# Kernel optimization log

Hardware: AMD Instinct MI355X
Metric: run time of the kernel (lower is better)

The kernel has to match this reference:

```python
import jax, jax.numpy as jnp
import numpy as np

M = 8192          # flattened tokens (batch*seq)
IN_FEATURES = 4096
OUT_FEATURES = 4096


def setup_inputs() -> dict:
    key = jax.random.key(0)
    k1, k2, k3 = jax.random.split(key, 3)
    # int8-valued activations and weights, stored as int32 (values in [-128, 127])
    x = jax.random.randint(k1, (M, IN_FEATURES), -128, 128, dtype=jnp.int32)
    int_weight = jax.random.randint(k2, (OUT_FEATURES, IN_FEATURES), -128, 127, dtype=jnp.int32)
    bias = (jax.random.normal(k3, (OUT_FEATURES,), dtype=jnp.float32) * 0.02).astype(jnp.float16)
    return {"x": x, "int_weight": int_weight, "bias": bias}


def reference(x, int_weight, bias):
    # x.to(torch.int8); quik int8Matmul: int8 GEMM with int32 accumulation, out = x @ W^T
    x_i8 = x.astype(jnp.int8)
    w_i8 = int_weight.astype(jnp.int8)
    acc = jax.lax.dot_general(
        x_i8, w_i8,
        dimension_numbers=(((1,), (1,)), ((), ())),  # [M, K] x [N, K] -> [M, N]
        preferred_element_type=jnp.int32,
    )
    # .to(torch.float16) then bias add (fused epilogue target)
    return acc.astype(jnp.float16) + bias
```

## Files before the change

kernel.cpp:

```cpp
#include <hip/hip_runtime.h>

#define MDIM 8192
#define NDIM 4096
#define KDIM 4096
#define BM 256
#define BN 128
#define BK 64

typedef int v4i __attribute__((ext_vector_type(4)));
typedef int v16i __attribute__((ext_vector_type(16)));

__device__ __forceinline__ unsigned pack4(int x, int y, int z, int w) {
    return (unsigned)(x & 0xff) | ((unsigned)(y & 0xff) << 8) |
           ((unsigned)(z & 0xff) << 16) | ((unsigned)w << 24);
}

__global__ __launch_bounds__(256) void pack_i32_to_i8(const int* __restrict__ in,
                                                      unsigned* __restrict__ out) {
    const int i = blockIdx.x * 256 + threadIdx.x;
    const int4* p = (const int4*)in + (size_t)i * 4;
    int4 a = p[0], b = p[1], c = p[2], d = p[3];
    uint4 r;
    r.x = pack4(a.x, a.y, a.z, a.w);
    r.y = pack4(b.x, b.y, b.z, b.w);
    r.z = pack4(c.x, c.y, c.z, c.w);
    r.w = pack4(d.x, d.y, d.z, d.w);
    ((uint4*)out)[i] = r;
}

template <bool PACKED>
__global__ __launch_bounds__(256, 2) void gemm_i8(const char* __restrict__ Ap,
                                                  const char* __restrict__ Bp,
                                                  const int* __restrict__ A32,
                                                  const int* __restrict__ B32,
                                                  const _Float16* __restrict__ bias,
                                                  _Float16* __restrict__ out) {
    __shared__ char lds[24576];
    char* ldsA = lds;
    char* ldsB = lds + 16384;

    const int tid  = threadIdx.x;
    const int lane = tid & 63;
    const int wave = tid >> 6;
    const int bm0 = blockIdx.y * BM;
    const int bn0 = blockIdx.x * BN;

    int aoffs[4], boffs[2];
    char* adst[4];
    char* bdst[2];
#pragma unroll
    for (int r = 0; r < 4; ++r) {
        const int flat = (r * 4 + wave) * 1024 + lane * 16;
        const int row  = flat >> 6;
        const int fblk = ((flat >> 4) & 3) ^ ((row >> 1) & 3);
        aoffs[r] = (bm0 + row) * KDIM + fblk * 16;
        adst[r]  = ldsA + (r * 4 + wave) * 1024;
    }
#pragma unroll
    for (int r = 0; r < 2; ++r) {
        const int flat = (r * 4 + wave) * 1024 + lane * 16;
        const int row  = flat >> 6;
        const int fblk = ((flat >> 4) & 3) ^ ((row >> 1) & 3);
        boffs[r] = (bn0 + row) * KDIM + fblk * 16;
        bdst[r]  = ldsB + (r * 4 + wave) * 1024;
    }

    const int wr  = wave >> 1;
    const int wc  = wave & 1;
    const int l31 = lane & 31;
    const int kg  = lane >> 5;
    int aaddr[4][2], baddr[2][2];
#pragma unroll
    for (int mt = 0; mt < 4; ++mt) {
        const int row = wr * 128 + mt * 32 + l31;
        const int swz = (row >> 1) & 3;
#pragma unroll
        for (int ks = 0; ks < 2; ++ks) {
            const int kb = ks * 2 + kg;
            aaddr[mt][ks] = row * 64 + ((kb ^ swz) << 4);
        }
    }
#pragma unroll
    for (int nt = 0; nt < 2; ++nt) {
        const int row = wc * 64 + nt * 32 + l31;
        const int swz = (row >> 1) & 3;
#pragma unroll
        for (int ks = 0; ks < 2; ++ks) {
            const int kb = ks * 2 + kg;
            baddr[nt][ks] = 16384 + row * 64 + ((kb ^ swz) << 4);
        }
    }

    v16i acc[4][2];
#pragma unroll
    for (int mt = 0; mt < 4; ++mt)
#pragma unroll
        for (int nt = 0; nt < 2; ++nt)
#pragma unroll
            for (int i = 0; i < 16; ++i) acc[mt][nt][i] = 0;

    for (int k0 = 0; k0 < KDIM; k0 += BK) {
        if constexpr (PACKED) {
#pragma unroll
            for (int r = 0; r < 4; ++r) {
                __builtin_amdgcn_global_load_lds(
                    (__attribute__((address_space(1))) void*)(Ap + aoffs[r]),
                    (__attribute__((address_space(3))) void*)(adst[r]), 16, 0, 0);
                aoffs[r] += BK;
            }
#pragma unroll
            for (int r = 0; r < 2; ++r) {
                __builtin_amdgcn_global_load_lds(
                    (__attribute__((address_space(1))) void*)(Bp + boffs[r]),
                    (__attribute__((address_space(3))) void*)(bdst[r]), 16, 0, 0);
                boffs[r] += BK;
            }
        } else {
#pragma unroll
            for (int r = 0; r < 4; ++r) {
                const int flat = (r * 4 + wave) * 1024 + lane * 16;
                const int row  = flat >> 6;
                const int fblk = ((flat >> 4) & 3) ^ ((row >> 1) & 3);
                const int* src = A32 + (size_t)(bm0 + row) * KDIM + k0 + fblk * 16;
                int4 v0 = ((const int4*)src)[0], v1 = ((const int4*)src)[1];
                int4 v2 = ((const int4*)src)[2], v3 = ((const int4*)src)[3];
                uint4 pk;
                pk.x = pack4(v0.x, v0.y, v0.z, v0.w);
                pk.y = pack4(v1.x, v1.y, v1.z, v1.w);
                pk.z = pack4(v2.x, v2.y, v2.z, v2.w);
                pk.w = pack4(v3.x, v3.y, v3.z, v3.w);
                *(uint4*)(ldsA + flat) = pk;
            }
#pragma unroll
            for (int r = 0; r < 2; ++r) {
                const int flat = (r * 4 + wave) * 1024 + lane * 16;
                const int row  = flat >> 6;
                const int fblk = ((flat >> 4) & 3) ^ ((row >> 1) & 3);
                const int* src = B32 + (size_t)(bn0 + row) * KDIM + k0 + fblk * 16;
                int4 v0 = ((const int4*)src)[0], v1 = ((const int4*)src)[1];
                int4 v2 = ((const int4*)src)[2], v3 = ((const int4*)src)[3];
                uint4 pk;
                pk.x = pack4(v0.x, v0.y, v0.z, v0.w);
                pk.y = pack4(v1.x, v1.y, v1.z, v1.w);
                pk.z = pack4(v2.x, v2.y, v2.z, v2.w);
                pk.w = pack4(v3.x, v3.y, v3.z, v3.w);
                *(uint4*)(ldsB + flat) = pk;
            }
        }
        __syncthreads();

        v4i af[4][2], bf[2][2];
#pragma unroll
        for (int mt = 0; mt < 4; ++mt)
#pragma unroll
            for (int ks = 0; ks < 2; ++ks)
                af[mt][ks] = *(const v4i*)(lds + aaddr[mt][ks]);
#pragma unroll
        for (int nt = 0; nt < 2; ++nt)
#pragma unroll
            for (int ks = 0; ks < 2; ++ks)
                bf[nt][ks] = *(const v4i*)(lds + baddr[nt][ks]);

#pragma unroll
        for (int ks = 0; ks < 2; ++ks)
#pragma unroll
            for (int mt = 0; mt < 4; ++mt)
#pragma unroll
                for (int nt = 0; nt < 2; ++nt)
                    acc[mt][nt] = __builtin_amdgcn_mfma_i32_32x32x32_i8(
                        af[mt][ks], bf[nt][ks], acc[mt][nt], 0, 0, 0);

        __syncthreads();
    }

    const _Float16 bv0 = bias[bn0 + wc * 64 + l31];
    const _Float16 bv1 = bias[bn0 + wc * 64 + 32 + l31];
#pragma unroll
    for (int mt = 0; mt < 4; ++mt) {
#pragma unroll
        for (int nt = 0; nt < 2; ++nt) {
            const int gcol = bn0 + wc * 64 + nt * 32 + l31;
            const _Float16 bb = nt ? bv1 : bv0;
#pragma unroll
            for (int r = 0; r < 16; ++r) {
                const int rit  = (r & 3) + 8 * (r >> 2) + 4 * kg;
                const int grow = bm0 + wr * 128 + mt * 32 + rit;
                _Float16 h = (_Float16)(float)acc[mt][nt][r] + bb;
                out[(size_t)grow * NDIM + gcol] = h;
            }
        }
    }
}

extern "C" void kernel_launch(void* const* d_in, const int* in_sizes, int n_in,
                              void* d_out, int out_size, void* d_ws, size_t ws_size,
                              hipStream_t stream) {
    const int* x = (const int*)d_in[0];
    const int* w = (const int*)d_in[1];
    const _Float16* bias = (const _Float16*)d_in[2];
    _Float16* out = (_Float16*)d_out;

    const size_t xbytes = (size_t)MDIM * KDIM;
    const size_t wbytes = (size_t)NDIM * KDIM;

    if (ws_size >= xbytes + wbytes) {
        char* xp = (char*)d_ws;
        char* wp = xp + xbytes;
        pack_i32_to_i8<<<MDIM * KDIM / 16 / 256, 256, 0, stream>>>(x, (unsigned*)xp);
        pack_i32_to_i8<<<NDIM * KDIM / 16 / 256, 256, 0, stream>>>(w, (unsigned*)wp);
        gemm_i8<true><<<dim3(NDIM / BN, MDIM / BM), 256, 0, stream>>>(
            xp, wp, nullptr, nullptr, bias, out);
    } else {
        gemm_i8<false><<<dim3(NDIM / BN, MDIM / BM), 256, 0, stream>>>(
            nullptr, nullptr, x, w, bias, out);
    }
}
```

Before: 409.2 us.

## Double K tile, switch LDS to k-block-major layout, merge pack kernels

```diff
diff --git a/kernel.cpp b/kernel.cpp
--- a/kernel.cpp
+++ b/kernel.cpp
@@ -5,7 +5,7 @@
 #define KDIM 4096
 #define BM 256
 #define BN 128
-#define BK 64
+#define BK 128
 
 typedef int v4i __attribute__((ext_vector_type(4)));
 typedef int v16i __attribute__((ext_vector_type(16)));
@@ -15,17 +15,25 @@
            ((unsigned)(z & 0xff) << 16) | ((unsigned)w << 24);
 }
 
-__global__ __launch_bounds__(256) void pack_i32_to_i8(const int* __restrict__ in,
-                                                      unsigned* __restrict__ out) {
+__global__ __launch_bounds__(256) void pack_pair(const int* __restrict__ x,
+                                                 const int* __restrict__ w,
+                                                 uint4* __restrict__ xp,
+                                                 uint4* __restrict__ wp) {
     const int i = blockIdx.x * 256 + threadIdx.x;
-    const int4* p = (const int4*)in + (size_t)i * 4;
+    const int xgroups = MDIM * KDIM / 16;
+    const int* src;
+    uint4* dst;
+    int g;
+    if (i < xgroups) { src = x; dst = xp; g = i; }
+    else             { src = w; dst = wp; g = i - xgroups; }
+    const int4* p = (const int4*)src + (size_t)g * 4;
     int4 a = p[0], b = p[1], c = p[2], d = p[3];
     uint4 r;
     r.x = pack4(a.x, a.y, a.z, a.w);
     r.y = pack4(b.x, b.y, b.z, b.w);
     r.z = pack4(c.x, c.y, c.z, c.w);
     r.w = pack4(d.x, d.y, d.z, d.w);
-    ((uint4*)out)[i] = r;
+    dst[g] = r;
 }
 
 template <bool PACKED>
@@ -35,9 +43,7 @@
                                                   const int* __restrict__ B32,
                                                   const _Float16* __restrict__ bias,
                                                   _Float16* __restrict__ out) {
-    __shared__ char lds[24576];
-    char* ldsA = lds;
-    char* ldsB = lds + 16384;
+    __shared__ char lds[49152];
 
     const int tid  = threadIdx.x;
     const int lane = tid & 63;
@@ -45,51 +51,37 @@
     const int bm0 = blockIdx.y * BM;
     const int bn0 = blockIdx.x * BN;
 
-    int aoffs[4], boffs[2];
-    char* adst[4];
-    char* bdst[2];
+    int aoffs[8], boffs[4];
+    char* adst[8];
+    char* bdst[4];
+#pragma unroll
+    for (int r = 0; r < 8; ++r) {
+        const int c  = r * 4 + wave;
+        const int kb = c >> 2;
+        const int rowb = (c & 3) * 64;
+        aoffs[r] = (bm0 + rowb + lane) * KDIM + kb * 16;
+        adst[r]  = lds + c * 1024;
+    }
 #pragma unroll
     for (int r = 0; r < 4; ++r) {
-        const int flat = (r * 4 + wave) * 1024 + lane * 16;
-        const int row  = flat >> 6;
-        const int fblk = ((flat >> 4) & 3) ^ ((row >> 1) & 3);
-        aoffs[r] = (bm0 + row) * KDIM + fblk * 16;
-        adst[r]  = ldsA + (r * 4 + wave) * 1024;
-    }
-#pragma unroll
-    for (int r = 0; r < 2; ++r) {
-        const int flat = (r * 4 + wave) * 1024 + lane * 16;
-        const int row  = flat >> 6;
-        const int fblk = ((flat >> 4) & 3) ^ ((row >> 1) & 3);
-        boffs[r] = (bn0 + row) * KDIM + fblk * 16;
-        bdst[r]  = ldsB + (r * 4 + wave) * 1024;
+        const int c  = r * 4 + wave;
+        const int kb = c >> 1;
+        const int rowb = (c & 1) * 64;
+        boffs[r] = (bn0 + rowb + lane) * KDIM + kb * 16;
+        bdst[r]  = lds + 32768 + c * 1024;
     }
 
     const int wr  = wave >> 1;
     const int wc  = wave & 1;
     const int l31 = lane & 31;
     const int kg  = lane >> 5;
-    int aaddr[4][2], baddr[2][2];
+    int abase[4], bbase[2];
 #pragma unroll
-    for (int mt = 0; mt < 4; ++mt) {
-        const int row = wr * 128 + mt * 32 + l31;
-        const int swz = (row >> 1) & 3;
+    for (int mt = 0; mt < 4; ++mt)
+        abase[mt] = kg * 4096 + (wr * 128 + mt * 32 + l31) * 16;
 #pragma unroll
-        for (int ks = 0; ks < 2; ++ks) {
-            const int kb = ks * 2 + kg;
-            aaddr[mt][ks] = row * 64 + ((kb ^ swz) << 4);
-        }
-    }
-#pragma unroll
-    for (int nt = 0; nt < 2; ++nt) {
-        const int row = wc * 64 + nt * 32 + l31;
-        const int swz = (row >> 1) & 3;
-#pragma unroll
-        for (int ks = 0; ks < 2; ++ks) {
-            const int kb = ks * 2 + kg;
-            baddr[nt][ks] = 16384 + row * 64 + ((kb ^ swz) << 4);
-        }
-    }
+    for (int nt = 0; nt < 2; ++nt)
+        bbase[nt] = 32768 + kg * 2048 + (wc * 64 + nt * 32 + l31) * 16;
 
     v16i acc[4][2];
 #pragma unroll
@@ -102,14 +94,14 @@
     for (int k0 = 0; k0 < KDIM; k0 += BK) {
         if constexpr (PACKED) {
 #pragma unroll
-            for (int r = 0; r < 4; ++r) {
+            for (int r = 0; r < 8; ++r) {
                 __builtin_amdgcn_global_load_lds(
                     (__attribute__((address_space(1))) void*)(Ap + aoffs[r]),
                     (__attribute__((address_space(3))) void*)(adst[r]), 16, 0, 0);
                 aoffs[r] += BK;
             }
 #pragma unroll
-            for (int r = 0; r < 2; ++r) {
+            for (int r = 0; r < 4; ++r) {
                 __builtin_amdgcn_global_load_lds(
                     (__attribute__((address_space(1))) void*)(Bp + boffs[r]),
                     (__attribute__((address_space(3))) void*)(bdst[r]), 16, 0, 0);
@@ -117,58 +109,48 @@
             }
         } else {
 #pragma unroll
-            for (int r = 0; r < 4; ++r) {
-                const int flat = (r * 4 + wave) * 1024 + lane * 16;
-                const int row  = flat >> 6;
-                const int fblk = ((flat >> 4) & 3) ^ ((row >> 1) & 3);
-                const int* src = A32 + (size_t)(bm0 + row) * KDIM + k0 + fblk * 16;
-                int4 v0 = ((const int4*)src)[0], v1 = ((const int4*)src)[1];
-                int4 v2 = ((const int4*)src)[2], v3 = ((const int4*)src)[3];
+            for (int r = 0; r < 8; ++r) {
+                const int4* s = (const int4*)(A32 + (size_t)aoffs[r]);
+                int4 v0 = s[0], v1 = s[1], v2 = s[2], v3 = s[3];
                 uint4 pk;
                 pk.x = pack4(v0.x, v0.y, v0.z, v0.w);
                 pk.y = pack4(v1.x, v1.y, v1.z, v1.w);
                 pk.z = pack4(v2.x, v2.y, v2.z, v2.w);
                 pk.w = pack4(v3.x, v3.y, v3.z, v3.w);
-                *(uint4*)(ldsA + flat) = pk;
+                *(uint4*)(adst[r] + lane * 16) = pk;
+                aoffs[r] += BK;
             }
 #pragma unroll
-            for (int r = 0; r < 2; ++r) {
-                const int flat = (r * 4 + wave) * 1024 + lane * 16;
-                const int row  = flat >> 6;
-                const int fblk = ((flat >> 4) & 3) ^ ((row >> 1) & 3);
-                const int* src = B32 + (size_t)(bn0 + row) * KDIM + k0 + fblk * 16;
-                int4 v0 = ((const int4*)src)[0], v1 = ((const int4*)src)[1];
-                int4 v2 = ((const int4*)src)[2], v3 = ((const int4*)src)[3];
+            for (int r = 0; r < 4; ++r) {
+                const int4* s = (const int4*)(B32 + (size_t)boffs[r]);
+                int4 v0 = s[0], v1 = s[1], v2 = s[2], v3 = s[3];
                 uint4 pk;
                 pk.x = pack4(v0.x, v0.y, v0.z, v0.w);
                 pk.y = pack4(v1.x, v1.y, v1.z, v1.w);
                 pk.z = pack4(v2.x, v2.y, v2.z, v2.w);
                 pk.w = pack4(v3.x, v3.y, v3.z, v3.w);
-                *(uint4*)(ldsB + flat) = pk;
+                *(uint4*)(bdst[r] + lane * 16) = pk;
+                boffs[r] += BK;
             }
         }
         __syncthreads();
 
-        v4i af[4][2], bf[2][2];
 #pragma unroll
-        for (int mt = 0; mt < 4; ++mt)
+        for (int ks = 0; ks < 4; ++ks) {
+            v4i af[4], bf[2];
 #pragma unroll
-            for (int ks = 0; ks < 2; ++ks)
-                af[mt][ks] = *(const v4i*)(lds + aaddr[mt][ks]);
+            for (int mt = 0; mt < 4; ++mt)
+                af[mt] = *(const v4i*)(lds + abase[mt] + ks * 8192);
 #pragma unroll
-        for (int nt = 0; nt < 2; ++nt)
-#pragma unroll
-            for (int ks = 0; ks < 2; ++ks)
-                bf[nt][ks] = *(const v4i*)(lds + baddr[nt][ks]);
-
-#pragma unroll
-        for (int ks = 0; ks < 2; ++ks)
+            for (int nt = 0; nt < 2; ++nt)
+                bf[nt] = *(const v4i*)(lds + bbase[nt] + ks * 4096);
 #pragma unroll
             for (int mt = 0; mt < 4; ++mt)
 #pragma unroll
                 for (int nt = 0; nt < 2; ++nt)
                     acc[mt][nt] = __builtin_amdgcn_mfma_i32_32x32x32_i8(
-                        af[mt][ks], bf[nt][ks], acc[mt][nt], 0, 0, 0);
+                        af[mt], bf[nt], acc[mt][nt], 0, 0, 0);
+        }
 
         __syncthreads();
     }
@@ -206,8 +188,8 @@
     if (ws_size >= xbytes + wbytes) {
         char* xp = (char*)d_ws;
         char* wp = xp + xbytes;
-        pack_i32_to_i8<<<MDIM * KDIM / 16 / 256, 256, 0, stream>>>(x, (unsigned*)xp);
-        pack_i32_to_i8<<<NDIM * KDIM / 16 / 256, 256, 0, stream>>>(w, (unsigned*)wp);
+        pack_pair<<<(MDIM + NDIM) * KDIM / 16 / 256, 256, 0, stream>>>(
+            x, w, (uint4*)xp, (uint4*)wp);
         gemm_i8<true><<<dim3(NDIM / BN, MDIM / BM), 256, 0, stream>>>(
             xp, wp, nullptr, nullptr, bias, out);
     } else {
```

New measurement: 518.3 us. 1.27x slower.
